# Kernel tuning notes

Hardware: AMD Instinct MI355X
Metric: run time of the kernel (lower is better)

The kernel has to match this reference:

```python
import jax, jax.numpy as jnp
import numpy as np

N = 500_000   # total nodes
B = 500       # number of graphs
C = 128       # channels


def setup_inputs() -> dict:
    key = jax.random.key(0)
    ks = jax.random.split(key, 10)
    node_embeddings = jax.random.normal(ks[0], (N, C), dtype=jnp.float32)
    latent_embeddings = jax.random.normal(ks[1], (B, C), dtype=jnp.float32)
    groups = jnp.sort(jax.random.randint(ks[2], (N,), 0, B)).astype(jnp.int32)
    # params (PyTorch Linear stored here as [in, out] matrices; same math)
    s = 1.0 / np.sqrt(C)
    attn_w = jax.random.normal(ks[3], (C, 1), dtype=jnp.float32) * s  # xavier-ish
    w_w = jax.random.normal(ks[4], (C, 1), dtype=jnp.float32) * s
    w_b = jnp.zeros((1,), dtype=jnp.float32)
    f1_w = jax.random.normal(ks[5], (C, C), dtype=jnp.float32) * s
    f1_b = jnp.zeros((C,), dtype=jnp.float32)
    f2_w = jax.random.normal(ks[6], (C, 1), dtype=jnp.float32) * s
    f2_b = jnp.zeros((1,), dtype=jnp.float32)
    return {
        "node_embeddings": node_embeddings,
        "latent_embeddings": latent_embeddings,
        "attn_w": attn_w, "w_w": w_w, "w_b": w_b,
        "f1_w": f1_w, "f1_b": f1_b, "f2_w": f2_w, "f2_b": f2_b,
        "groups": groups, "num_segments": B,
    }


def reference(node_embeddings, latent_embeddings, attn_w, w_w, w_b,
              f1_w, f1_b, f2_w, f2_b, groups, num_segments):
    # gather per-node context (faithful to original: indexes node table by graph id)
    ctx = node_embeddings[groups]            # [N, C]
    lat = latent_embeddings[groups]          # [N, C]
    alpha = jax.nn.sigmoid(ctx @ w_w + w_b)  # [N, 1]
    f_out = jax.nn.relu(lat @ f1_w + f1_b) @ f2_w + f2_b  # [N, 1]
    attn = alpha * f_out + (1.0 - alpha) * attn_w.T       # [N, C]
    scores = jnp.sum(node_embeddings * attn, axis=1, keepdims=True)  # [N, 1]
    scores = jnp.exp(scores - jnp.max(scores, axis=0, keepdims=True))
    denom = jax.ops.segment_sum(scores, groups, num_segments=num_segments)[groups]
    scores = scores / denom
    graph_embeddings = jax.ops.segment_sum(node_embeddings * scores, groups,
                                           num_segments=num_segments)  # [B, C]
    return graph_embeddings
```

## Files before the change

### kernel.cpp

```cpp
#include <hip/hip_runtime.h>
#include <math.h>

#define C 128
#define SPLIT 4
#define PSTRIDE (C + 4)

__global__ void k_bounds(const int* __restrict__ groups, int n, int b,
                         int* __restrict__ start) {
    int i = blockIdx.x * blockDim.x + threadIdx.x;
    if (i >= n) return;
    int g = groups[i];
    int gp = (i == 0) ? -1 : groups[i - 1];
    for (int gg = gp + 1; gg <= g; ++gg) start[gg] = i;
    if (i == n - 1)
        for (int gg = g + 1; gg <= b; ++gg) start[gg] = n;
}

__global__ __launch_bounds__(256, 4)
void k_attn_part(const float* __restrict__ node, const float* __restrict__ latent,
                 const float* __restrict__ attn_w, const float* __restrict__ w_w,
                 const float* __restrict__ w_b, const float* __restrict__ f1_w,
                 const float* __restrict__ f1_b, const float* __restrict__ f2_w,
                 const float* __restrict__ f2_b, const int* __restrict__ start,
                 float* __restrict__ part) {
    const int bid = blockIdx.x;
    const int g = bid >> 2;
    const int q = bid & 3;
    const int tid = threadIdx.x;
    const int lane = tid & 63;
    const int wv = tid >> 6;

    __shared__ float lds_lat[C];
    __shared__ float lds_attn[C];
    __shared__ float red[4];
    __shared__ float wacc[4][C];
    __shared__ float wm[4], wd[4];

    if (tid < C) lds_lat[tid] = latent[(size_t)g * C + tid];
    __syncthreads();
    if (tid < C) {
        float ap = node[(size_t)g * C + tid] * w_w[tid];
        float h = f1_b[tid];
        #pragma unroll 8
        for (int in = 0; in < C; ++in)
            h = fmaf(lds_lat[in], f1_w[in * C + tid], h);
        h = fmaxf(h, 0.f);
        float fp = h * f2_w[tid];
        #pragma unroll
        for (int off = 32; off >= 1; off >>= 1) {
            ap += __shfl_xor(ap, off);
            fp += __shfl_xor(fp, off);
        }
        if (lane == 0) { red[wv * 2] = ap; red[wv * 2 + 1] = fp; }
    }
    __syncthreads();
    if (tid < C) {
        float a_sum = red[0] + red[2];
        float f_sum = red[1] + red[3];
        float alpha = 1.f / (1.f + __expf(-(a_sum + w_b[0])));
        float fout = f_sum + f2_b[0];
        lds_attn[tid] = alpha * fout + (1.f - alpha) * attn_w[tid];
    }
    __syncthreads();

    const int lo = start[g], hi = start[g + 1];
    const int len = hi - lo;
    const int s0 = lo + (len * q) / SPLIT;
    const int s1 = lo + (len * (q + 1)) / SPLIT;

    const int half = lane >> 5;
    const int cl = lane & 31;
    const float4 av = *(const float4*)&lds_attn[cl * 4];

    float m = -INFINITY, denom = 0.f;
    float4 acc = make_float4(0.f, 0.f, 0.f, 0.f);

    for (int base = s0 + wv * 8; base < s1; base += 32) {
        float4 r[4];
        #pragma unroll
        for (int j = 0; j < 4; ++j) {
            int row = base + 2 * j + half;
            int rc = row < s1 ? row : (s1 - 1);
            r[j] = *(const float4*)&node[(size_t)rc * C + cl * 4];
        }
        float s[4];
        #pragma unroll
        for (int j = 0; j < 4; ++j)
            s[j] = fmaf(r[j].x, av.x, fmaf(r[j].y, av.y,
                    fmaf(r[j].z, av.z, r[j].w * av.w)));

        float k0, k1;
        {
            float ka = (lane & 1) ? s[1] : s[0];
            float sa = (lane & 1) ? s[0] : s[1];
            float kb = (lane & 1) ? s[3] : s[2];
            float sb = (lane & 1) ? s[2] : s[3];
            k0 = ka + __shfl_xor(sa, 1);
            k1 = kb + __shfl_xor(sb, 1);
        }
        float k;
        {
            float ka = (lane & 2) ? k1 : k0;
            float sa = (lane & 2) ? k0 : k1;
            k = ka + __shfl_xor(sa, 2);
        }
        k += __shfl_xor(k, 4);
        k += __shfl_xor(k, 8);
        k += __shfl_xor(k, 16);
        int rown = base + 2 * (lane & 3) + half;
        k = (rown < s1) ? k : -INFINITY;

        float mx = k;
        mx = fmaxf(mx, __shfl_xor(mx, 1));
        mx = fmaxf(mx, __shfl_xor(mx, 2));
        mx = fmaxf(mx, __shfl_xor(mx, 32));
        float mb = fmaxf(m, mx);
        float scale = __expf(m - mb);
        float p = __expf(k - mb);

        float ps = p;
        ps += __shfl_xor(ps, 1);
        ps += __shfl_xor(ps, 2);
        ps += __shfl_xor(ps, 32);
        denom = fmaf(denom, scale, ps);

        float pe[4], po[4];
        #pragma unroll
        for (int t = 0; t < 4; ++t) {
            pe[t] = __shfl(p, t);
            po[t] = __shfl(p, 32 + t);
        }
        acc.x *= scale; acc.y *= scale; acc.z *= scale; acc.w *= scale;
        #pragma unroll
        for (int j = 0; j < 4; ++j) {
            float pj = half ? po[j] : pe[j];
            acc.x = fmaf(pj, r[j].x, acc.x);
            acc.y = fmaf(pj, r[j].y, acc.y);
            acc.z = fmaf(pj, r[j].z, acc.z);
            acc.w = fmaf(pj, r[j].w, acc.w);
        }
        m = mb;
    }

    acc.x += __shfl_xor(acc.x, 32);
    acc.y += __shfl_xor(acc.y, 32);
    acc.z += __shfl_xor(acc.z, 32);
    acc.w += __shfl_xor(acc.w, 32);

    if (lane == 0) { wm[wv] = m; wd[wv] = denom; }
    if (lane < 32) {
        wacc[wv][cl * 4 + 0] = acc.x;
        wacc[wv][cl * 4 + 1] = acc.y;
        wacc[wv][cl * 4 + 2] = acc.z;
        wacc[wv][cl * 4 + 3] = acc.w;
    }
    __syncthreads();

    if (tid < C) {
        float M = fmaxf(fmaxf(wm[0], wm[1]), fmaxf(wm[2], wm[3]));
        float D = 0.f, A = 0.f;
        #pragma unroll
        for (int w = 0; w < 4; ++w) {
            float sc = (wm[w] == -INFINITY) ? 0.f : __expf(wm[w] - M);
            D = fmaf(wd[w], sc, D);
            A = fmaf(wacc[w][tid], sc, A);
        }
        size_t pb = (size_t)bid * PSTRIDE;
        if (tid == 0) { part[pb] = M; part[pb + 1] = D; }
        part[pb + 4 + tid] = A;
    }
}

__global__ void k_merge(const float* __restrict__ part, float* __restrict__ out) {
    int g = blockIdx.x;
    int c = threadIdx.x;
    float M = -INFINITY;
    #pragma unroll
    for (int q = 0; q < SPLIT; ++q)
        M = fmaxf(M, part[(size_t)(g * SPLIT + q) * PSTRIDE]);
    float D = 0.f, A = 0.f;
    #pragma unroll
    for (int q = 0; q < SPLIT; ++q) {
        size_t pb = (size_t)(g * SPLIT + q) * PSTRIDE;
        float mq = part[pb];
        float sc = (mq == -INFINITY) ? 0.f : __expf(mq - M);
        D = fmaf(part[pb + 1], sc, D);
        A = fmaf(part[pb + 4 + c], sc, A);
    }
    out[(size_t)g * C + c] = (D > 0.f) ? (A / D) : 0.f;
}

extern "C" void kernel_launch(void* const* d_in, const int* in_sizes, int n_in,
                              void* d_out, int out_size, void* d_ws, size_t ws_size,
                              hipStream_t stream) {
    const float* node   = (const float*)d_in[0];
    const float* latent = (const float*)d_in[1];
    const float* attn_w = (const float*)d_in[2];
    const float* w_w    = (const float*)d_in[3];
    const float* w_b    = (const float*)d_in[4];
    const float* f1_w   = (const float*)d_in[5];
    const float* f1_b   = (const float*)d_in[6];
    const float* f2_w   = (const float*)d_in[7];
    const float* f2_b   = (const float*)d_in[8];
    const int*   groups = (const int*)d_in[9];

    const int n = in_sizes[9];
    const int b = in_sizes[1] / C;

    int*   start = (int*)d_ws;
    float* part  = (float*)((char*)d_ws + 4096);

    k_bounds<<<(n + 255) / 256, 256, 0, stream>>>(groups, n, b, start);
    k_attn_part<<<b * SPLIT, 256, 0, stream>>>(node, latent, attn_w, w_w, w_b,
                                               f1_w, f1_b, f2_w, f2_b, start, part);
    k_merge<<<b, C, 0, stream>>>(part, (float*)d_out);
}
```

Before: 55.72 us.

## Move per-graph attention vector computation into bounds kernel, store to workspace

```diff
diff --git a/kernel.cpp b/kernel.cpp
--- a/kernel.cpp
+++ b/kernel.cpp
@@ -5,23 +5,70 @@
 #define SPLIT 4
 #define PSTRIDE (C + 4)
 
-__global__ void k_bounds(const int* __restrict__ groups, int n, int b,
-                         int* __restrict__ start) {
-    int i = blockIdx.x * blockDim.x + threadIdx.x;
-    if (i >= n) return;
-    int g = groups[i];
-    int gp = (i == 0) ? -1 : groups[i - 1];
-    for (int gg = gp + 1; gg <= g; ++gg) start[gg] = i;
-    if (i == n - 1)
-        for (int gg = g + 1; gg <= b; ++gg) start[gg] = n;
+__global__ void k_prep(const int* __restrict__ groups, int n, int b, int nbb,
+                       const float* __restrict__ node,
+                       const float* __restrict__ latent,
+                       const float* __restrict__ attn_w,
+                       const float* __restrict__ w_w,
+                       const float* __restrict__ w_b,
+                       const float* __restrict__ f1_w,
+                       const float* __restrict__ f1_b,
+                       const float* __restrict__ f2_w,
+                       const float* __restrict__ f2_b,
+                       int* __restrict__ start, float* __restrict__ attnv) {
+    __shared__ float lds_lat[C];
+    __shared__ float red[4];
+
+    if ((int)blockIdx.x < nbb) {
+        int i = blockIdx.x * blockDim.x + threadIdx.x;
+        if (i >= n) return;
+        int g = groups[i];
+        int gp = (i == 0) ? -1 : groups[i - 1];
+        for (int gg = gp + 1; gg <= g; ++gg) start[gg] = i;
+        if (i == n - 1)
+            for (int gg = g + 1; gg <= b; ++gg) start[gg] = n;
+        return;
+    }
+
+    const int g = blockIdx.x - nbb;
+    const int tid = threadIdx.x;
+    const int lane = tid & 63;
+    const int wv = tid >> 6;
+
+    if (tid < C) lds_lat[tid] = latent[(size_t)g * C + tid];
+    __syncthreads();
+    if (tid < C) {
+        float ap = node[(size_t)g * C + tid] * w_w[tid];
+        float h0 = 0.f, h1 = 0.f;
+        #pragma unroll 8
+        for (int in = 0; in < C / 2; ++in)
+            h0 = fmaf(lds_lat[in], f1_w[in * C + tid], h0);
+        #pragma unroll 8
+        for (int in = C / 2; in < C; ++in)
+            h1 = fmaf(lds_lat[in], f1_w[in * C + tid], h1);
+        float h = fmaxf(h0 + h1 + f1_b[tid], 0.f);
+        float fp = h * f2_w[tid];
+        #pragma unroll
+        for (int off = 32; off >= 1; off >>= 1) {
+            ap += __shfl_xor(ap, off);
+            fp += __shfl_xor(fp, off);
+        }
+        if (lane == 0) { red[wv * 2] = ap; red[wv * 2 + 1] = fp; }
+    }
+    __syncthreads();
+    if (tid < C) {
+        float a_sum = red[0] + red[2];
+        float f_sum = red[1] + red[3];
+        float alpha = 1.f / (1.f + __expf(-(a_sum + w_b[0])));
+        float fout = f_sum + f2_b[0];
+        attnv[(size_t)g * C + tid] = alpha * fout + (1.f - alpha) * attn_w[tid];
+    }
 }
 
 __global__ __launch_bounds__(256, 4)
-void k_attn_part(const float* __restrict__ node, const float* __restrict__ latent,
-                 const float* __restrict__ attn_w, const float* __restrict__ w_w,
-                 const float* __restrict__ w_b, const float* __restrict__ f1_w,
-                 const float* __restrict__ f1_b, const float* __restrict__ f2_w,
-                 const float* __restrict__ f2_b, const int* __restrict__ start,
+void k_attn_part(const float* __restrict__ node,
+                 const float* __restrict__ attnv,
+                 const int* __restrict__ start,
                  float* __restrict__ part) {
     const int bid = blockIdx.x;
     const int g = bid >> 2;
@@ -30,38 +77,8 @@
     const int lane = tid & 63;
     const int wv = tid >> 6;
 
-    __shared__ float lds_lat[C];
-    __shared__ float lds_attn[C];
-    __shared__ float red[4];
     __shared__ float wacc[4][C];
     __shared__ float wm[4], wd[4];
-
-    if (tid < C) lds_lat[tid] = latent[(size_t)g * C + tid];
-    __syncthreads();
-    if (tid < C) {
-        float ap = node[(size_t)g * C + tid] * w_w[tid];
-        float h = f1_b[tid];
-        #pragma unroll 8
-        for (int in = 0; in < C; ++in)
-            h = fmaf(lds_lat[in], f1_w[in * C + tid], h);
-        h = fmaxf(h, 0.f);
-        float fp = h * f2_w[tid];
-        #pragma unroll
-        for (int off = 32; off >= 1; off >>= 1) {
-            ap += __shfl_xor(ap, off);
-            fp += __shfl_xor(fp, off);
-        }
-        if (lane == 0) { red[wv * 2] = ap; red[wv * 2 + 1] = fp; }
-    }
-    __syncthreads();
-    if (tid < C) {
-        float a_sum = red[0] + red[2];
-        float f_sum = red[1] + red[3];
-        float alpha = 1.f / (1.f + __expf(-(a_sum + w_b[0])));
-        float fout = f_sum + f2_b[0];
-        lds_attn[tid] = alpha * fout + (1.f - alpha) * attn_w[tid];
-    }
-    __syncthreads();
 
     const int lo = start[g], hi = start[g + 1];
     const int len = hi - lo;
@@ -70,7 +87,7 @@
 
     const int half = lane >> 5;
     const int cl = lane & 31;
-    const float4 av = *(const float4*)&lds_attn[cl * 4];
+    const float4 av = *(const float4*)&attnv[(size_t)g * C + cl * 4];
 
     float m = -INFINITY, denom = 0.f;
     float4 acc = make_float4(0.f, 0.f, 0.f, 0.f);
@@ -208,10 +225,13 @@
     const int b = in_sizes[1] / C;
 
     int*   start = (int*)d_ws;
-    float* part  = (float*)((char*)d_ws + 4096);
-
-    k_bounds<<<(n + 255) / 256, 256, 0, stream>>>(groups, n, b, start);
-    k_attn_part<<<b * SPLIT, 256, 0, stream>>>(node, latent, attn_w, w_w, w_b,
-                                               f1_w, f1_b, f2_w, f2_b, start, part);
+    float* attnv = (float*)((char*)d_ws + 4096);
+    float* part  = (float*)((char*)d_ws + 4096 + 1048576);
+
+    const int nbb = (n + 255) / 256;
+    k_prep<<<nbb + b, 256, 0, stream>>>(groups, n, b, nbb, node, latent,
+                                        attn_w, w_w, w_b, f1_w, f1_b, f2_w, f2_b,
+                                        start, attnv);
+    k_attn_part<<<b * SPLIT, 256, 0, stream>>>(node, attnv, start, part);
     k_merge<<<b, C, 0, stream>>>(part, (float*)d_out);
 }
```

After: 52.65 us. -5.5%, faster.
